# Optimization experiments

Measured on AMD Instinct MI355X. Metric: run time of the kernel, lower is better.

The kernel has to match this reference:

```python
import jax, jax.numpy as jnp
import numpy as np

B, C, D, H, W = 2, 256, 16, 64, 64


def _conv1x1(x, w, b):
    # 1x1x1 Conv3d == pointwise channel matmul. x: [B,C,D,H,W], w: [Cout,Cin], b: [Cout]
    return jnp.einsum('bcdhw,oc->bodhw', x, w) + b[None, :, None, None, None]


def setup_inputs() -> dict:
    key = jax.random.key(0)
    ks = jax.random.split(key, 12)
    wscale = 1.0 / np.sqrt(C)  # keep pre-softmax logits in a sane range
    inp = {
        'eeg_input': jax.random.normal(ks[0], (B, C, D, H, W), jnp.float32),
        'image_input': jax.random.normal(ks[1], (B, C, D, H, W), jnp.float32),
        'q_w': jax.random.normal(ks[2], (C, C), jnp.float32) * wscale,
        'q_b': jnp.zeros((C,), jnp.float32),
        'k_w': jax.random.normal(ks[3], (C, C), jnp.float32) * wscale,
        'k_b': jnp.zeros((C,), jnp.float32),
        'v_w': jax.random.normal(ks[4], (C, C), jnp.float32) * wscale,
        'v_b': jnp.zeros((C,), jnp.float32),
        'attn_w': jax.random.normal(ks[5], (C, C), jnp.float32) * wscale,
        'attn_b': jnp.zeros((C,), jnp.float32),
        'out_w': jax.random.normal(ks[6], (C, C), jnp.float32) * wscale,
        'out_b': jnp.zeros((C,), jnp.float32),
    }
    return inp


def reference(eeg_input, image_input, q_w, q_b, k_w, k_b, v_w, v_b,
              attn_w, attn_b, out_w, out_b):
    q = _conv1x1(eeg_input, q_w, q_b)      # [B,C,D,H,W]
    k = _conv1x1(image_input, k_w, k_b)    # [B,C,D,H,W]
    v = _conv1x1(image_input, v_w, v_b)    # [B,C,D,H,W]
    # torch.matmul(q, k.transpose(-2,-1)): contract over W -> scores [B,C,D,H,H]
    scores = jax.nn.softmax(jnp.einsum('bcdhw,bcdxw->bcdhx', q, k), axis=-1)
    wv = jnp.einsum('bcdhx,bcdxw->bcdhw', scores, v)  # [B,C,D,H,W]
    a = jax.nn.relu(_conv1x1(wv, attn_w, attn_b))
    return jax.nn.relu(_conv1x1(a, out_w, out_b))
```

## Files before the change

### kernel.cpp

```cpp
#include <hip/hip_runtime.h>

#define CC   256
#define DHWC 65536
#define NBC  2

typedef __attribute__((ext_vector_type(8))) short bf16x8;
typedef __attribute__((ext_vector_type(4))) short bf16x4;
typedef __attribute__((ext_vector_type(4))) float f32x4;

__device__ __forceinline__ short f2bf(float x) {
    unsigned u = __builtin_bit_cast(unsigned, x);
    unsigned r = (u + 0x7fffu + ((u >> 16) & 1u)) >> 16;
    return (short)r;
}
__device__ __forceinline__ float bf2f(short h) {
    unsigned u = ((unsigned)(unsigned short)h) << 16;
    return __builtin_bit_cast(float, u);
}

__device__ __forceinline__ int swz(int r, int c) {
    return (r * 128 + c * 2) ^ ((r & 7) << 4);
}
__device__ __forceinline__ int vswz(int r, int c) {
    return (r * 128 + c * 2) ^ (((r ^ (r >> 3)) & 7) << 4);
}
__device__ __forceinline__ int swz512(int s, int k) {
    return (s * 512 + k * 2) ^ ((s & 7) << 4);
}

__global__ void prep_w_kernel(const float* __restrict__ q_w, const float* __restrict__ k_w,
                              const float* __restrict__ v_w, const float* __restrict__ attn_w,
                              const float* __restrict__ out_w, short* __restrict__ wsp)
{
    const int l  = threadIdx.x;
    const int fo = blockIdx.x;
    const int t  = blockIdx.y;
    const int m  = blockIdx.z;
    const float* w = (m == 0) ? q_w : (m == 1) ? k_w : (m == 2) ? v_w
                   : (m == 3) ? attn_w : out_w;
    short* whi = wsp + (size_t)m * 131072;
    short* wlo = whi + 65536;

    const int o = fo * 16 + (l & 15);
    const int k = t * 32 + (l >> 4) * 8;

    bf16x8 hv, lv;
    #pragma unroll
    for (int r = 0; r < 8; ++r) {
        const float x = w[o * 256 + k + r];
        const short h = f2bf(x);
        hv[r] = h;
        lv[r] = f2bf(x - bf2f(h));
    }
    const int idx = (fo * 8 + t) * 64 + l;
    *(bf16x8*)(whi + idx * 8) = hv;
    *(bf16x8*)(wlo + idx * 8) = lv;
}

__global__ __launch_bounds__(512, 4) void conv_mfma_kernel(
    const float* __restrict__ x, const short* __restrict__ whi,
    const short* __restrict__ wlo, const float* __restrict__ bias,
    float* __restrict__ out, const int do_relu)
{
    __shared__ bf16x8 xhi[2][512];
    __shared__ bf16x8 xlo[2][512];

    const int tid  = threadIdx.x;
    const int lane = tid & 63;
    const int wave = tid >> 6;
    const size_t boff = (size_t)blockIdx.y * ((size_t)CC * DHWC);
    const int sT = blockIdx.x * 64;
    const float* xb = x + boff + sT;
    const bf16x8* whf = (const bf16x8*)whi;
    const bf16x8* wlf = (const bf16x8*)wlo;

    f32x4 acc[2][4];
    #pragma unroll
    for (int f = 0; f < 2; ++f)
        #pragma unroll
        for (int j = 0; j < 4; ++j)
            acc[f][j] = (f32x4){0.f, 0.f, 0.f, 0.f};

    const int s_l = tid & 63;
    const int k8  = tid >> 6;

    float xr[8];
    #pragma unroll
    for (int r = 0; r < 8; ++r)
        xr[r] = xb[(size_t)(k8 * 8 + r) * DHWC + s_l];
    {
        bf16x8 hv, lv;
        #pragma unroll
        for (int r = 0; r < 8; ++r) {
            const short h = f2bf(xr[r]);
            hv[r] = h;
            lv[r] = f2bf(xr[r] - bf2f(h));
        }
        *(bf16x8*)((char*)xhi[0] + swz(s_l, k8 * 8)) = hv;
        *(bf16x8*)((char*)xlo[0] + swz(s_l, k8 * 8)) = lv;
    }

    #pragma unroll
    for (int t = 0; t < 4; ++t) {
        if (t < 3) {
            #pragma unroll
            for (int r = 0; r < 8; ++r)
                xr[r] = xb[(size_t)((t + 1) * 64 + k8 * 8 + r) * DHWC + s_l];
        }
        __syncthreads();

        const char* bhib = (const char*)xhi[t & 1];
        const char* blob = (const char*)xlo[t & 1];
        #pragma unroll
        for (int kk = 0; kk < 2; ++kk) {
            bf16x8 a1h[2], a1l[2];
            #pragma unroll
            for (int f = 0; f < 2; ++f) {
                const int idx = ((wave * 2 + f) * 8 + 2 * t + kk) * 64 + lane;
                a1h[f] = whf[idx];
                a1l[f] = wlf[idx];
            }
            bf16x8 bh[4], bl[4];
            #pragma unroll
            for (int j = 0; j < 4; ++j) {
                const int s = j * 16 + (lane & 15);
                const int k = kk * 32 + (lane >> 4) * 8;
                bh[j] = *(const bf16x8*)(bhib + swz(s, k));
                bl[j] = *(const bf16x8*)(blob + swz(s, k));
            }
            #pragma unroll
            for (int f = 0; f < 2; ++f)
                #pragma unroll
                for (int j = 0; j < 4; ++j) {
                    f32x4 c = acc[f][j];
                    c = __builtin_amdgcn_mfma_f32_16x16x32_bf16(a1h[f], bh[j], c, 0, 0, 0);
                    c = __builtin_amdgcn_mfma_f32_16x16x32_bf16(a1h[f], bl[j], c, 0, 0, 0);
                    c = __builtin_amdgcn_mfma_f32_16x16x32_bf16(a1l[f], bh[j], c, 0, 0, 0);
                    acc[f][j] = c;
                }
        }

        if (t < 3) {
            bf16x8 hv, lv;
            #pragma unroll
            for (int r = 0; r < 8; ++r) {
                const short h = f2bf(xr[r]);
                hv[r] = h;
                lv[r] = f2bf(xr[r] - bf2f(h));
            }
            *(bf16x8*)((char*)xhi[(t + 1) & 1] + swz(s_l, k8 * 8)) = hv;
            *(bf16x8*)((char*)xlo[(t + 1) & 1] + swz(s_l, k8 * 8)) = lv;
        }
    }

    float* ob = out + boff + sT;
    const int n_l = lane & 15;
    const int m4  = (lane >> 4) * 4;
    #pragma unroll
    for (int f = 0; f < 2; ++f) {
        #pragma unroll
        for (int r = 0; r < 4; ++r) {
            const int o = wave * 32 + f * 16 + m4 + r;
            const float bv = bias[o];
            #pragma unroll
            for (int j = 0; j < 4; ++j) {
                float val = acc[f][j][r] + bv;
                if (do_relu) val = fmaxf(val, 0.f);
                ob[(size_t)o * DHWC + j * 16 + n_l] = val;
            }
        }
    }
}

__global__ __launch_bounds__(512, 4) void kv_conv_kernel(
    const float* __restrict__ img,
    const short* __restrict__ wkhi, const short* __restrict__ wklo,
    const short* __restrict__ wvhi, const short* __restrict__ wvlo,
    const float* __restrict__ kb, const float* __restrict__ vb,
    float* __restrict__ kout, short* __restrict__ vout)
{
    __shared__ bf16x8 xhi[2][512];
    __shared__ bf16x8 xlo[2][512];

    const int tid  = threadIdx.x;
    const int lane = tid & 63;
    const int wave = tid >> 6;
    const size_t boff = (size_t)blockIdx.y * ((size_t)CC * DHWC);
    const int sT = blockIdx.x * 64;
    const float* xb = img + boff + sT;
    const bf16x8* wkhf = (const bf16x8*)wkhi;
    const bf16x8* wklf = (const bf16x8*)wklo;
    const bf16x8* wvhf = (const bf16x8*)wvhi;
    const bf16x8* wvlf = (const bf16x8*)wvlo;

    f32x4 acck[2][4], accv[2][4];
    #pragma unroll
    for (int f = 0; f < 2; ++f)
        #pragma unroll
        for (int j = 0; j < 4; ++j) {
            acck[f][j] = (f32x4){0.f, 0.f, 0.f, 0.f};
            accv[f][j] = (f32x4){0.f, 0.f, 0.f, 0.f};
        }

    const int s_l = tid & 63;
    const int k8  = tid >> 6;

    float xr[8];
    #pragma unroll
    for (int r = 0; r < 8; ++r)
        xr[r] = xb[(size_t)(k8 * 8 + r) * DHWC + s_l];
    {
        bf16x8 hv, lv;
        #pragma unroll
        for (int r = 0; r < 8; ++r) {
            const short h = f2bf(xr[r]);
            hv[r] = h;
            lv[r] = f2bf(xr[r] - bf2f(h));
        }
        *(bf16x8*)((char*)xhi[0] + swz(s_l, k8 * 8)) = hv;
        *(bf16x8*)((char*)xlo[0] + swz(s_l, k8 * 8)) = lv;
    }

    #pragma unroll
    for (int t = 0; t < 4; ++t) {
        if (t < 3) {
            #pragma unroll
            for (int r = 0; r < 8; ++r)
                xr[r] = xb[(size_t)((t + 1) * 64 + k8 * 8 + r) * DHWC + s_l];
        }
        __syncthreads();

        const char* bhib = (const char*)xhi[t & 1];
        const char* blob = (const char*)xlo[t & 1];
        #pragma unroll
        for (int kk = 0; kk < 2; ++kk) {
            bf16x8 akh[2], akl[2], avh[2], avl[2];
            #pragma unroll
            for (int f = 0; f < 2; ++f) {
                const int idx = ((wave * 2 + f) * 8 + 2 * t + kk) * 64 + lane;
                akh[f] = wkhf[idx];
                akl[f] = wklf[idx];
                avh[f] = wvhf[idx];
                avl[f] = wvlf[idx];
            }
            #pragma unroll
            for (int j = 0; j < 4; ++j) {
                const int s = j * 16 + (lane & 15);
                const int k = kk * 32 + (lane >> 4) * 8;
                const bf16x8 bh = *(const bf16x8*)(bhib + swz(s, k));
                const bf16x8 bl = *(const bf16x8*)(blob + swz(s, k));
                #pragma unroll
                for (int f = 0; f < 2; ++f) {
                    f32x4 c = acck[f][j];
                    c = __builtin_amdgcn_mfma_f32_16x16x32_bf16(akh[f], bh, c, 0, 0, 0);
                    c = __builtin_amdgcn_mfma_f32_16x16x32_bf16(akh[f], bl, c, 0, 0, 0);
                    c = __builtin_amdgcn_mfma_f32_16x16x32_bf16(akl[f], bh, c, 0, 0, 0);
                    acck[f][j] = c;
                    f32x4 d = accv[f][j];
                    d = __builtin_amdgcn_mfma_f32_16x16x32_bf16(avh[f], bh, d, 0, 0, 0);
                    d = __builtin_amdgcn_mfma_f32_16x16x32_bf16(avh[f], bl, d, 0, 0, 0);
                    d = __builtin_amdgcn_mfma_f32_16x16x32_bf16(avl[f], bh, d, 0, 0, 0);
                    accv[f][j] = d;
                }
            }
        }

        if (t < 3) {
            bf16x8 hv, lv;
            #pragma unroll
            for (int r = 0; r < 8; ++r) {
                const short h = f2bf(xr[r]);
                hv[r] = h;
                lv[r] = f2bf(xr[r] - bf2f(h));
            }
            *(bf16x8*)((char*)xhi[(t + 1) & 1] + swz(s_l, k8 * 8)) = hv;
            *(bf16x8*)((char*)xlo[(t + 1) & 1] + swz(s_l, k8 * 8)) = lv;
        }
    }

    float* ko = kout + boff + sT;
    short* vo = vout + boff + sT;
    const int n_l = lane & 15;
    const int m4  = (lane >> 4) * 4;
    #pragma unroll
    for (int f = 0; f < 2; ++f) {
        #pragma unroll
        for (int r = 0; r < 4; ++r) {
            const int o = wave * 32 + f * 16 + m4 + r;
            const float kbv = kb[o];
            const float vbv = vb[o];
            #pragma unroll
            for (int j = 0; j < 4; ++j) {
                ko[(size_t)o * DHWC + j * 16 + n_l] = acck[f][j][r] + kbv;
                vo[(size_t)o * DHWC + j * 16 + n_l] = f2bf(accv[f][j][r] + vbv);
            }
        }
    }
}

__global__ __launch_bounds__(256, 4) void attn_mfma_kernel(
    const float* q, const float* __restrict__ kg,
    const short* __restrict__ vsh, float* wv)
{
    __shared__ char lds[40960];
    const int QHI = 0, QLO = 8192, KHI = 16384, KLO = 24576, VT = 32768;

    const int tid  = threadIdx.x;
    const int lane = tid & 63;
    const int wsx  = tid >> 6;
    const size_t base = (size_t)blockIdx.x * 4096;

    {
        const int r  = tid >> 2;
        const int cb = (tid & 3) * 16;
        #pragma unroll
        for (int half = 0; half < 2; ++half) {
            const int c = cb + half * 8;
            const float4 qa = *(const float4*)(q  + base + r * 64 + c);
            const float4 qb = *(const float4*)(q  + base + r * 64 + c + 4);
            const float4 ka = *(const float4*)(kg + base + r * 64 + c);
            const float4 kb = *(const float4*)(kg + base + r * 64 + c + 4);
            bf16x8 qh, ql, kh, kl;
            #pragma unroll
            for (int e = 0; e < 4; ++e) {
                float xq = ((const float*)&qa)[e];
                short h = f2bf(xq); qh[e] = h; ql[e] = f2bf(xq - bf2f(h));
                xq = ((const float*)&qb)[e];
                h = f2bf(xq); qh[e + 4] = h; ql[e + 4] = f2bf(xq - bf2f(h));
                float xk = ((const float*)&ka)[e];
                h = f2bf(xk); kh[e] = h; kl[e] = f2bf(xk - bf2f(h));
                xk = ((const float*)&kb)[e];
                h = f2bf(xk); kh[e + 4] = h; kl[e + 4] = f2bf(xk - bf2f(h));
            }
            const int off = swz(r, c);
            *(bf16x8*)(lds + QHI + off) = qh;
            *(bf16x8*)(lds + QLO + off) = ql;
            *(bf16x8*)(lds + KHI + off) = kh;
            *(bf16x8*)(lds + KLO + off) = kl;
        }
        const short* vpl = vsh + base;
        const int x0 = (tid >> 4) * 4;
        const int w0 = (tid & 15) * 4;
        bf16x4 vr[4];
        #pragma unroll
        for (int i = 0; i < 4; ++i)
            vr[i] = *(const bf16x4*)(vpl + (x0 + i) * 64 + w0);
        #pragma unroll
        for (int j = 0; j < 4; ++j) {
            bf16x4 tv;
            #pragma unroll
            for (int i = 0; i < 4; ++i) tv[i] = vr[i][j];
            *(bf16x4*)(lds + VT + vswz(w0 + j, x0)) = tv;
        }
    }
    __syncthreads();

    f32x4 acc[4];
    #pragma unroll
    for (int j = 0; j < 4; ++j) acc[j] = (f32x4){0.f, 0.f, 0.f, 0.f};

    const int arow = wsx * 16 + (lane & 15);
    #pragma unroll
    for (int kk = 0; kk < 2; ++kk) {
        const int kcol = kk * 32 + (lane >> 4) * 8;
        const bf16x8 aqh = *(const bf16x8*)(lds + QHI + swz(arow, kcol));
        const bf16x8 aql = *(const bf16x8*)(lds + QLO + swz(arow, kcol));
        #pragma unroll
        for (int j = 0; j < 4; ++j) {
            const int brow = j * 16 + (lane & 15);
            const bf16x8 bkh = *(const bf16x8*)(lds + KHI + swz(brow, kcol));
            const bf16x8 bkl = *(const bf16x8*)(lds + KLO + swz(brow, kcol));
            f32x4 c = acc[j];
            c = __builtin_amdgcn_mfma_f32_16x16x32_bf16(aqh, bkh, c, 0, 0, 0);
            c = __builtin_amdgcn_mfma_f32_16x16x32_bf16(aqh, bkl, c, 0, 0, 0);
            c = __builtin_amdgcn_mfma_f32_16x16x32_bf16(aql, bkh, c, 0, 0, 0);
            acc[j] = c;
        }
    }

    float p[4][4], invs[4];
    #pragma unroll
    for (int r = 0; r < 4; ++r) {
        float m = fmaxf(fmaxf(acc[0][r], acc[1][r]), fmaxf(acc[2][r], acc[3][r]));
        m = fmaxf(m, __shfl_xor(m, 1));
        m = fmaxf(m, __shfl_xor(m, 2));
        m = fmaxf(m, __shfl_xor(m, 4));
        m = fmaxf(m, __shfl_xor(m, 8));
        float s = 0.f;
        #pragma unroll
        for (int j = 0; j < 4; ++j) { p[j][r] = __expf(acc[j][r] - m); s += p[j][r]; }
        s += __shfl_xor(s, 1);
        s += __shfl_xor(s, 2);
        s += __shfl_xor(s, 4);
        s += __shfl_xor(s, 8);
        invs[r] = 1.f / s;
    }

    __syncthreads();

    #pragma unroll
    for (int r = 0; r < 4; ++r) {
        const int row = wsx * 16 + (lane >> 4) * 4 + r;
        #pragma unroll
        for (int j = 0; j < 4; ++j) {
            const int col = j * 16 + (lane & 15);
            *(short*)(lds + QHI + swz(row, col)) = f2bf(p[j][r]);
        }
    }
    __syncthreads();

    f32x4 o_[4];
    #pragma unroll
    for (int j = 0; j < 4; ++j) o_[j] = (f32x4){0.f, 0.f, 0.f, 0.f};

    #pragma unroll
    for (int kk = 0; kk < 2; ++kk) {
        const int kcol = kk * 32 + (lane >> 4) * 8;
        const bf16x8 aph = *(const bf16x8*)(lds + QHI + swz(arow, kcol));
        #pragma unroll
        for (int j = 0; j < 4; ++j) {
            const int brow = j * 16 + (lane & 15);
            const bf16x8 bvh = *(const bf16x8*)(lds + VT + vswz(brow, kcol));
            o_[j] = __builtin_amdgcn_mfma_f32_16x16x32_bf16(aph, bvh, o_[j], 0, 0, 0);
        }
    }

    #pragma unroll
    for (int r = 0; r < 4; ++r) {
        const int h = wsx * 16 + (lane >> 4) * 4 + r;
        #pragma unroll
        for (int j = 0; j < 4; ++j)
            wv[base + (size_t)h * 64 + j * 16 + (lane & 15)] = o_[j][r] * invs[r];
    }
}

__global__ __launch_bounds__(512, 4) void tail_fused_kernel(
    const float* __restrict__ x,
    const short* __restrict__ w1hi, const short* __restrict__ w1lo,
    const float* __restrict__ b1,
    const short* __restrict__ w2hi, const short* __restrict__ w2lo,
    const float* __restrict__ b2,
    float* __restrict__ out)
{
    __shared__ char lds[65536];
    const int tid  = threadIdx.x;
    const int lane = tid & 63;
    const int wave = tid >> 6;
    const size_t boff = (size_t)blockIdx.y * ((size_t)CC * DHWC);
    const int sT = blockIdx.x * 64;
    const float* xb = x + boff + sT;
    const bf16x8* w1hf = (const bf16x8*)w1hi;
    const bf16x8* w1lf = (const bf16x8*)w1lo;

    f32x4 acc[2][4];
    #pragma unroll
    for (int f = 0; f < 2; ++f)
        #pragma unroll
        for (int j = 0; j < 4; ++j)
            acc[f][j] = (f32x4){0.f, 0.f, 0.f, 0.f};

    const int s_l = tid & 63;
    const int k8  = tid >> 6;

    float xr[8];
    #pragma unroll
    for (int r = 0; r < 8; ++r)
        xr[r] = xb[(size_t)(k8 * 8 + r) * DHWC + s_l];
    {
        bf16x8 hv, lv;
        #pragma unroll
        for (int r = 0; r < 8; ++r) {
            const short h = f2bf(xr[r]);
            hv[r] = h;
            lv[r] = f2bf(xr[r] - bf2f(h));
        }
        *(bf16x8*)(lds + swz(s_l, k8 * 8)) = hv;
        *(bf16x8*)(lds + 8192 + swz(s_l, k8 * 8)) = lv;
    }

    #pragma unroll
    for (int t = 0; t < 4; ++t) {
        if (t < 3) {
            #pragma unroll
            for (int r = 0; r < 8; ++r)
                xr[r] = xb[(size_t)((t + 1) * 64 + k8 * 8 + r) * DHWC + s_l];
        }
        __syncthreads();

        const char* bhib = lds + (t & 1) * 16384;
        const char* blob = bhib + 8192;
        #pragma unroll
        for (int kk = 0; kk < 2; ++kk) {
            bf16x8 a1h[2], a1l[2];
            #pragma unroll
            for (int f = 0; f < 2; ++f) {
                const int idx = ((wave * 2 + f) * 8 + 2 * t + kk) * 64 + lane;
                a1h[f] = w1hf[idx];
                a1l[f] = w1lf[idx];
            }
            bf16x8 bh[4], bl[4];
            #pragma unroll
            for (int j = 0; j < 4; ++j) {
                const int s = j * 16 + (lane & 15);
                const int k = kk * 32 + (lane >> 4) * 8;
                bh[j] = *(const bf16x8*)(bhib + swz(s, k));
                bl[j] = *(const bf16x8*)(blob + swz(s, k));
            }
            #pragma unroll
            for (int f = 0; f < 2; ++f)
                #pragma unroll
                for (int j = 0; j < 4; ++j) {
                    f32x4 c = acc[f][j];
                    c = __builtin_amdgcn_mfma_f32_16x16x32_bf16(a1h[f], bh[j], c, 0, 0, 0);
                    c = __builtin_amdgcn_mfma_f32_16x16x32_bf16(a1h[f], bl[j], c, 0, 0, 0);
                    c = __builtin_amdgcn_mfma_f32_16x16x32_bf16(a1l[f], bh[j], c, 0, 0, 0);
                    acc[f][j] = c;
                }
        }

        if (t < 3) {
            bf16x8 hv, lv;
            #pragma unroll
            for (int r = 0; r < 8; ++r) {
                const short h = f2bf(xr[r]);
                hv[r] = h;
                lv[r] = f2bf(xr[r] - bf2f(h));
            }
            *(bf16x8*)(lds + ((t + 1) & 1) * 16384 + swz(s_l, k8 * 8)) = hv;
            *(bf16x8*)(lds + ((t + 1) & 1) * 16384 + 8192 + swz(s_l, k8 * 8)) = lv;
        }
    }

    __syncthreads();
    #pragma unroll
    for (int f = 0; f < 2; ++f) {
        #pragma unroll
        for (int r = 0; r < 4; ++r) {
            const int o = wave * 32 + f * 16 + (lane >> 4) * 4 + r;
            const float bv = b1[o];
            #pragma unroll
            for (int j = 0; j < 4; ++j) {
                const int s = j * 16 + (lane & 15);
                const float val = fmaxf(acc[f][j][r] + bv, 0.f);
                const short h = f2bf(val);
                const int off = swz512(s, o);
                *(short*)(lds + off) = h;
                *(short*)(lds + 32768 + off) = f2bf(val - bf2f(h));
            }
        }
    }
    __syncthreads();

    f32x4 acc2[2][4];
    #pragma unroll
    for (int f = 0; f < 2; ++f)
        #pragma unroll
        for (int j = 0; j < 4; ++j)
            acc2[f][j] = (f32x4){0.f, 0.f, 0.f, 0.f};

    const bf16x8* w2hf = (const bf16x8*)w2hi;
    const bf16x8* w2lf = (const bf16x8*)w2lo;
    #pragma unroll
    for (int t2 = 0; t2 < 8; ++t2) {
        bf16x8 a2h[2], a2l[2];
        #pragma unroll
        for (int f = 0; f < 2; ++f) {
            const int idx = ((wave * 2 + f) * 8 + t2) * 64 + lane;
            a2h[f] = w2hf[idx];
            a2l[f] = w2lf[idx];
        }
        bf16x8 bh[4], bl[4];
        #pragma unroll
        for (int j = 0; j < 4; ++j) {
            const int s = j * 16 + (lane & 15);
            const int k = t2 * 32 + (lane >> 4) * 8;
            const int off = swz512(s, k);
            bh[j] = *(const bf16x8*)(lds + off);
            bl[j] = *(const bf16x8*)(lds + 32768 + off);
        }
        #pragma unroll
        for (int f = 0; f < 2; ++f)
            #pragma unroll
            for (int j = 0; j < 4; ++j) {
                f32x4 c = acc2[f][j];
                c = __builtin_amdgcn_mfma_f32_16x16x32_bf16(a2h[f], bh[j], c, 0, 0, 0);
                c = __builtin_amdgcn_mfma_f32_16x16x32_bf16(a2h[f], bl[j], c, 0, 0, 0);
                c = __builtin_amdgcn_mfma_f32_16x16x32_bf16(a2l[f], bh[j], c, 0, 0, 0);
                acc2[f][j] = c;
            }
    }

    float* ob = out + boff + sT;
    const int n_l = lane & 15;
    const int m4  = (lane >> 4) * 4;
    #pragma unroll
    for (int f = 0; f < 2; ++f) {
        #pragma unroll
        for (int r = 0; r < 4; ++r) {
            const int o = wave * 32 + f * 16 + m4 + r;
            const float bv = b2[o];
            #pragma unroll
            for (int j = 0; j < 4; ++j) {
                const float val = fmaxf(acc2[f][j][r] + bv, 0.f);
                ob[(size_t)o * DHWC + j * 16 + n_l] = val;
            }
        }
    }
}

extern "C" void kernel_launch(void* const* d_in, const int* in_sizes, int n_in,
                              void* d_out, int out_size, void* d_ws, size_t ws_size,
                              hipStream_t stream)
{
    const float* eeg    = (const float*)d_in[0];
    const float* img    = (const float*)d_in[1];
    const float* q_w    = (const float*)d_in[2];
    const float* q_b    = (const float*)d_in[3];
    const float* k_w    = (const float*)d_in[4];
    const float* k_b    = (const float*)d_in[5];
    const float* v_w    = (const float*)d_in[6];
    const float* v_b    = (const float*)d_in[7];
    const float* attn_w = (const float*)d_in[8];
    const float* attn_b = (const float*)d_in[9];
    const float* out_w  = (const float*)d_in[10];
    const float* out_b  = (const float*)d_in[11];

    const size_t N = (size_t)NBC * CC * DHWC;
    float* qbuf = (float*)d_ws;
    float* kbuf = qbuf + N;
    short* wsp  = (short*)(kbuf + N);
    short* vsh  = (short*)d_out;
    float* outp = (float*)d_out;

    hipLaunchKernelGGL(prep_w_kernel, dim3(16, 8, 5), dim3(64), 0, stream,
                       q_w, k_w, v_w, attn_w, out_w, wsp);

    const dim3 cgrid(DHWC / 64, NBC);

    hipLaunchKernelGGL(conv_mfma_kernel, cgrid, dim3(512), 0, stream,
                       eeg, wsp, wsp + 65536, q_b, qbuf, 0);

    hipLaunchKernelGGL(kv_conv_kernel, cgrid, dim3(512), 0, stream,
                       img, wsp + 131072, wsp + 131072 + 65536,
                       wsp + 2 * 131072, wsp + 2 * 131072 + 65536,
                       k_b, v_b, kbuf, vsh);

    hipLaunchKernelGGL(attn_mfma_kernel, dim3(NBC * CC * 16), dim3(256), 0, stream,
                       qbuf, kbuf, vsh, qbuf);

    hipLaunchKernelGGL(tail_fused_kernel, cgrid, dim3(512), 0, stream,
                       qbuf, wsp + 3 * 131072, wsp + 3 * 131072 + 65536, attn_b,
                       wsp + 4 * 131072, wsp + 4 * 131072 + 65536, out_b, outp);
}
```

Before: 417.4 us.

## Widen conv tiles to 128 spatial with 1024-thread blocks; drop lo-part in tail stage-2

The three pointwise-conv kernels now use 1024-thread blocks over 128 spatial positions, and each of the 16 waves owns 16 output channels instead of 32. Each weight fragment is reused across 8 spatial sub-tiles instead of 4, while each LDS activation tile is shared by twice as many waves. In the tail kernel, the intermediate ReLU activation is stored only as a bf16 hi part, so the second conv does two MFMAs per tile instead of three, trading some accuracy for less LDS traffic and compute. The larger block raises register pressure per thread and may reduce occupancy with a 64KB LDS allocation.

After: 410.1 us. About the same (-1.8%).

```diff
diff --git a/kernel.cpp b/kernel.cpp
--- a/kernel.cpp
+++ b/kernel.cpp
@@ -57,32 +57,28 @@
     *(bf16x8*)(wlo + idx * 8) = lv;
 }
 
-__global__ __launch_bounds__(512, 4) void conv_mfma_kernel(
+__global__ __launch_bounds__(1024, 4) void conv_mfma_kernel(
     const float* __restrict__ x, const short* __restrict__ whi,
     const short* __restrict__ wlo, const float* __restrict__ bias,
     float* __restrict__ out, const int do_relu)
 {
-    __shared__ bf16x8 xhi[2][512];
-    __shared__ bf16x8 xlo[2][512];
+    __shared__ char lds[65536];
 
     const int tid  = threadIdx.x;
     const int lane = tid & 63;
     const int wave = tid >> 6;
     const size_t boff = (size_t)blockIdx.y * ((size_t)CC * DHWC);
-    const int sT = blockIdx.x * 64;
+    const int sT = blockIdx.x * 128;
     const float* xb = x + boff + sT;
     const bf16x8* whf = (const bf16x8*)whi;
     const bf16x8* wlf = (const bf16x8*)wlo;
 
-    f32x4 acc[2][4];
-    #pragma unroll
-    for (int f = 0; f < 2; ++f)
-        #pragma unroll
-        for (int j = 0; j < 4; ++j)
-            acc[f][j] = (f32x4){0.f, 0.f, 0.f, 0.f};
-
-    const int s_l = tid & 63;
-    const int k8  = tid >> 6;
+    f32x4 acc[8];
+    #pragma unroll
+    for (int j = 0; j < 8; ++j) acc[j] = (f32x4){0.f, 0.f, 0.f, 0.f};
+
+    const int s_l = tid & 127;
+    const int k8  = tid >> 7;
 
     float xr[8];
     #pragma unroll
@@ -96,8 +92,9 @@
             hv[r] = h;
             lv[r] = f2bf(xr[r] - bf2f(h));
         }
-        *(bf16x8*)((char*)xhi[0] + swz(s_l, k8 * 8)) = hv;
-        *(bf16x8*)((char*)xlo[0] + swz(s_l, k8 * 8)) = lv;
+        const int off = swz(s_l, k8 * 8);
+        *(bf16x8*)(lds + off) = hv;
+        *(bf16x8*)(lds + 16384 + off) = lv;
     }
 
     #pragma unroll
@@ -109,35 +106,25 @@
         }
         __syncthreads();
 
-        const char* bhib = (const char*)xhi[t & 1];
-        const char* blob = (const char*)xlo[t & 1];
+        const char* bhib = lds + (t & 1) * 32768;
+        const char* blob = bhib + 16384;
         #pragma unroll
         for (int kk = 0; kk < 2; ++kk) {
-            bf16x8 a1h[2], a1l[2];
-            #pragma unroll
-            for (int f = 0; f < 2; ++f) {
-                const int idx = ((wave * 2 + f) * 8 + 2 * t + kk) * 64 + lane;
-                a1h[f] = whf[idx];
-                a1l[f] = wlf[idx];
-            }
-            bf16x8 bh[4], bl[4];
-            #pragma unroll
-            for (int j = 0; j < 4; ++j) {
+            const int idx = (wave * 8 + 2 * t + kk) * 64 + lane;
+            const bf16x8 a1h = whf[idx];
+            const bf16x8 a1l = wlf[idx];
+            #pragma unroll
+            for (int j = 0; j < 8; ++j) {
                 const int s = j * 16 + (lane & 15);
                 const int k = kk * 32 + (lane >> 4) * 8;
-                bh[j] = *(const bf16x8*)(bhib + swz(s, k));
-                bl[j] = *(const bf16x8*)(blob + swz(s, k));
-            }
-            #pragma unroll
-            for (int f = 0; f < 2; ++f)
-                #pragma unroll
-                for (int j = 0; j < 4; ++j) {
-                    f32x4 c = acc[f][j];
-                    c = __builtin_amdgcn_mfma_f32_16x16x32_bf16(a1h[f], bh[j], c, 0, 0, 0);
-                    c = __builtin_amdgcn_mfma_f32_16x16x32_bf16(a1h[f], bl[j], c, 0, 0, 0);
-                    c = __builtin_amdgcn_mfma_f32_16x16x32_bf16(a1l[f], bh[j], c, 0, 0, 0);
-                    acc[f][j] = c;
-                }
+                const bf16x8 bh = *(const bf16x8*)(bhib + swz(s, k));
+                const bf16x8 bl = *(const bf16x8*)(blob + swz(s, k));
+                f32x4 c = acc[j];
+                c = __builtin_amdgcn_mfma_f32_16x16x32_bf16(a1h, bh, c, 0, 0, 0);
+                c = __builtin_amdgcn_mfma_f32_16x16x32_bf16(a1h, bl, c, 0, 0, 0);
+                c = __builtin_amdgcn_mfma_f32_16x16x32_bf16(a1l, bh, c, 0, 0, 0);
+                acc[j] = c;
+            }
         }
 
         if (t < 3) {
@@ -148,8 +135,9 @@
                 hv[r] = h;
                 lv[r] = f2bf(xr[r] - bf2f(h));
             }
-            *(bf16x8*)((char*)xhi[(t + 1) & 1] + swz(s_l, k8 * 8)) = hv;
-            *(bf16x8*)((char*)xlo[(t + 1) & 1] + swz(s_l, k8 * 8)) = lv;
+            const int off = ((t + 1) & 1) * 32768 + swz(s_l, k8 * 8);
+            *(bf16x8*)(lds + off) = hv;
+            *(bf16x8*)(lds + 16384 + off) = lv;
         }
     }
 
@@ -157,53 +145,47 @@
     const int n_l = lane & 15;
     const int m4  = (lane >> 4) * 4;
     #pragma unroll
-    for (int f = 0; f < 2; ++f) {
-        #pragma unroll
-        for (int r = 0; r < 4; ++r) {
-            const int o = wave * 32 + f * 16 + m4 + r;
-            const float bv = bias[o];
-            #pragma unroll
-            for (int j = 0; j < 4; ++j) {
-                float val = acc[f][j][r] + bv;
-                if (do_relu) val = fmaxf(val, 0.f);
-                ob[(size_t)o * DHWC + j * 16 + n_l] = val;
-            }
-        }
-    }
-}
-
-__global__ __launch_bounds__(512, 4) void kv_conv_kernel(
+    for (int r = 0; r < 4; ++r) {
+        const int o = wave * 16 + m4 + r;
+        const float bv = bias[o];
+        #pragma unroll
+        for (int j = 0; j < 8; ++j) {
+            float val = acc[j][r] + bv;
+            if (do_relu) val = fmaxf(val, 0.f);
+            ob[(size_t)o * DHWC + j * 16 + n_l] = val;
+        }
+    }
+}
+
+__global__ __launch_bounds__(1024, 4) void kv_conv_kernel(
     const float* __restrict__ img,
     const short* __restrict__ wkhi, const short* __restrict__ wklo,
     const short* __restrict__ wvhi, const short* __restrict__ wvlo,
     const float* __restrict__ kb, const float* __restrict__ vb,
     float* __restrict__ kout, short* __restrict__ vout)
 {
-    __shared__ bf16x8 xhi[2][512];
-    __shared__ bf16x8 xlo[2][512];
+    __shared__ char lds[65536];
 
     const int tid  = threadIdx.x;
     const int lane = tid & 63;
     const int wave = tid >> 6;
     const size_t boff = (size_t)blockIdx.y * ((size_t)CC * DHWC);
-    const int sT = blockIdx.x * 64;
+    const int sT = blockIdx.x * 128;
     const float* xb = img + boff + sT;
     const bf16x8* wkhf = (const bf16x8*)wkhi;
     const bf16x8* wklf = (const bf16x8*)wklo;
     const bf16x8* wvhf = (const bf16x8*)wvhi;
     const bf16x8* wvlf = (const bf16x8*)wvlo;
 
-    f32x4 acck[2][4], accv[2][4];
-    #pragma unroll
-    for (int f = 0; f < 2; ++f)
-        #pragma unroll
-        for (int j = 0; j < 4; ++j) {
-            acck[f][j] = (f32x4){0.f, 0.f, 0.f, 0.f};
-            accv[f][j] = (f32x4){0.f, 0.f, 0.f, 0.f};
-        }
-
-    const int s_l = tid & 63;
-    const int k8  = tid >> 6;
+    f32x4 acck[8], accv[8];
+    #pragma unroll
+    for (int j = 0; j < 8; ++j) {
+        acck[j] = (f32x4){0.f, 0.f, 0.f, 0.f};
+        accv[j] = (f32x4){0.f, 0.f, 0.f, 0.f};
+    }
+
+    const int s_l = tid & 127;
+    const int k8  = tid >> 7;
 
     float xr[8];
     #pragma unroll
@@ -217,8 +199,9 @@
             hv[r] = h;
             lv[r] = f2bf(xr[r] - bf2f(h));
         }
-        *(bf16x8*)((char*)xhi[0] + swz(s_l, k8 * 8)) = hv;
-        *(bf16x8*)((char*)xlo[0] + swz(s_l, k8 * 8)) = lv;
+        const int off = swz(s_l, k8 * 8);
+        *(bf16x8*)(lds + off) = hv;
+        *(bf16x8*)(lds + 16384 + off) = lv;
     }
 
     #pragma unroll
@@ -230,38 +213,31 @@
         }
         __syncthreads();
 
-        const char* bhib = (const char*)xhi[t & 1];
-        const char* blob = (const char*)xlo[t & 1];
+        const char* bhib = lds + (t & 1) * 32768;
+        const char* blob = bhib + 16384;
         #pragma unroll
         for (int kk = 0; kk < 2; ++kk) {
-            bf16x8 akh[2], akl[2], avh[2], avl[2];
-            #pragma unroll
-            for (int f = 0; f < 2; ++f) {
-                const int idx = ((wave * 2 + f) * 8 + 2 * t + kk) * 64 + lane;
-                akh[f] = wkhf[idx];
-                akl[f] = wklf[idx];
-                avh[f] = wvhf[idx];
-                avl[f] = wvlf[idx];
-            }
-            #pragma unroll
-            for (int j = 0; j < 4; ++j) {
+            const int idx = (wave * 8 + 2 * t + kk) * 64 + lane;
+            const bf16x8 akh = wkhf[idx];
+            const bf16x8 akl = wklf[idx];
+            const bf16x8 avh = wvhf[idx];
+            const bf16x8 avl = wvlf[idx];
+            #pragma unroll
+            for (int j = 0; j < 8; ++j) {
                 const int s = j * 16 + (lane & 15);
                 const int k = kk * 32 + (lane >> 4) * 8;
                 const bf16x8 bh = *(const bf16x8*)(bhib + swz(s, k));
                 const bf16x8 bl = *(const bf16x8*)(blob + swz(s, k));
-                #pragma unroll
-                for (int f = 0; f < 2; ++f) {
-                    f32x4 c = acck[f][j];
-                    c = __builtin_amdgcn_mfma_f32_16x16x32_bf16(akh[f], bh, c, 0, 0, 0);
-                    c = __builtin_amdgcn_mfma_f32_16x16x32_bf16(akh[f], bl, c, 0, 0, 0);
-                    c = __builtin_amdgcn_mfma_f32_16x16x32_bf16(akl[f], bh, c, 0, 0, 0);
-                    acck[f][j] = c;
-                    f32x4 d = accv[f][j];
-                    d = __builtin_amdgcn_mfma_f32_16x16x32_bf16(avh[f], bh, d, 0, 0, 0);
-                    d = __builtin_amdgcn_mfma_f32_16x16x32_bf16(avh[f], bl, d, 0, 0, 0);
-                    d = __builtin_amdgcn_mfma_f32_16x16x32_bf16(avl[f], bh, d, 0, 0, 0);
-                    accv[f][j] = d;
-                }
+                f32x4 c = acck[j];
+                c = __builtin_amdgcn_mfma_f32_16x16x32_bf16(akh, bh, c, 0, 0, 0);
+                c = __builtin_amdgcn_mfma_f32_16x16x32_bf16(akh, bl, c, 0, 0, 0);
+                c = __builtin_amdgcn_mfma_f32_16x16x32_bf16(akl, bh, c, 0, 0, 0);
+                acck[j] = c;
+                f32x4 d = accv[j];
+                d = __builtin_amdgcn_mfma_f32_16x16x32_bf16(avh, bh, d, 0, 0, 0);
+                d = __builtin_amdgcn_mfma_f32_16x16x32_bf16(avh, bl, d, 0, 0, 0);
+                d = __builtin_amdgcn_mfma_f32_16x16x32_bf16(avl, bh, d, 0, 0, 0);
+                accv[j] = d;
             }
         }
 
@@ -273,8 +249,9 @@
                 hv[r] = h;
                 lv[r] = f2bf(xr[r] - bf2f(h));
             }
-            *(bf16x8*)((char*)xhi[(t + 1) & 1] + swz(s_l, k8 * 8)) = hv;
-            *(bf16x8*)((char*)xlo[(t + 1) & 1] + swz(s_l, k8 * 8)) = lv;
+            const int off = ((t + 1) & 1) * 32768 + swz(s_l, k8 * 8);
+            *(bf16x8*)(lds + off) = hv;
+            *(bf16x8*)(lds + 16384 + off) = lv;
         }
     }
 
@@ -283,17 +260,14 @@
     const int n_l = lane & 15;
     const int m4  = (lane >> 4) * 4;
     #pragma unroll
-    for (int f = 0; f < 2; ++f) {
-        #pragma unroll
-        for (int r = 0; r < 4; ++r) {
-            const int o = wave * 32 + f * 16 + m4 + r;
-            const float kbv = kb[o];
-            const float vbv = vb[o];
-            #pragma unroll
-            for (int j = 0; j < 4; ++j) {
-                ko[(size_t)o * DHWC + j * 16 + n_l] = acck[f][j][r] + kbv;
-                vo[(size_t)o * DHWC + j * 16 + n_l] = f2bf(accv[f][j][r] + vbv);
-            }
+    for (int r = 0; r < 4; ++r) {
+        const int o = wave * 16 + m4 + r;
+        const float kbv = kb[o];
+        const float vbv = vb[o];
+        #pragma unroll
+        for (int j = 0; j < 8; ++j) {
+            ko[(size_t)o * DHWC + j * 16 + n_l] = acck[j][r] + kbv;
+            vo[(size_t)o * DHWC + j * 16 + n_l] = f2bf(accv[j][r] + vbv);
         }
     }
 }
@@ -434,7 +408,7 @@
     }
 }
 
-__global__ __launch_bounds__(512, 4) void tail_fused_kernel(
+__global__ __launch_bounds__(1024, 4) void tail_fused_kernel(
     const float* __restrict__ x,
     const short* __restrict__ w1hi, const short* __restrict__ w1lo,
     const float* __restrict__ b1,
@@ -443,24 +417,22 @@
     float* __restrict__ out)
 {
     __shared__ char lds[65536];
+
     const int tid  = threadIdx.x;
     const int lane = tid & 63;
     const int wave = tid >> 6;
     const size_t boff = (size_t)blockIdx.y * ((size_t)CC * DHWC);
-    const int sT = blockIdx.x * 64;
+    const int sT = blockIdx.x * 128;
     const float* xb = x + boff + sT;
     const bf16x8* w1hf = (const bf16x8*)w1hi;
     const bf16x8* w1lf = (const bf16x8*)w1lo;
 
-    f32x4 acc[2][4];
-    #pragma unroll
-    for (int f = 0; f < 2; ++f)
-        #pragma unroll
-        for (int j = 0; j < 4; ++j)
-            acc[f][j] = (f32x4){0.f, 0.f, 0.f, 0.f};
-
-    const int s_l = tid & 63;
-    const int k8  = tid >> 6;
+    f32x4 acc[8];
+    #pragma unroll
+    for (int j = 0; j < 8; ++j) acc[j] = (f32x4){0.f, 0.f, 0.f, 0.f};
+
+    const int s_l = tid & 127;
+    const int k8  = tid >> 7;
 
     float xr[8];
     #pragma unroll
@@ -474,8 +446,9 @@
             hv[r] = h;
             lv[r] = f2bf(xr[r] - bf2f(h));
         }
-        *(bf16x8*)(lds + swz(s_l, k8 * 8)) = hv;
-        *(bf16x8*)(lds + 8192 + swz(s_l, k8 * 8)) = lv;
+        const int off = swz(s_l, k8 * 8);
+        *(bf16x8*)(lds + off) = hv;
+        *(bf16x8*)(lds + 16384 + off) = lv;
     }
 
     #pragma unroll
@@ -487,35 +460,25 @@
         }
         __syncthreads();
 
-        const char* bhib = lds + (t & 1) * 16384;
-        const char* blob = bhib + 8192;
+        const char* bhib = lds + (t & 1) * 32768;
+        const char* blob = bhib + 16384;
         #pragma unroll
         for (int kk = 0; kk < 2; ++kk) {
-            bf16x8 a1h[2], a1l[2];
-            #pragma unroll
-            for (int f = 0; f < 2; ++f) {
-                const int idx = ((wave * 2 + f) * 8 + 2 * t + kk) * 64 + lane;
-                a1h[f] = w1hf[idx];
-                a1l[f] = w1lf[idx];
-            }
-            bf16x8 bh[4], bl[4];
-            #pragma unroll
-            for (int j = 0; j < 4; ++j) {
+            const int idx = (wave * 8 + 2 * t + kk) * 64 + lane;
+            const bf16x8 a1h = w1hf[idx];
+            const bf16x8 a1l = w1lf[idx];
+            #pragma unroll
+            for (int j = 0; j < 8; ++j) {
                 const int s = j * 16 + (lane & 15);
                 const int k = kk * 32 + (lane >> 4) * 8;
-                bh[j] = *(const bf16x8*)(bhib + swz(s, k));
-                bl[j] = *(const bf16x8*)(blob + swz(s, k));
-            }
-            #pragma unroll
-            for (int f = 0; f < 2; ++f)
-                #pragma unroll
-                for (int j = 0; j < 4; ++j) {
-                    f32x4 c = acc[f][j];
-                    c = __builtin_amdgcn_mfma_f32_16x16x32_bf16(a1h[f], bh[j], c, 0, 0, 0);
-                    c = __builtin_amdgcn_mfma_f32_16x16x32_bf16(a1h[f], bl[j], c, 0, 0, 0);
-                    c = __builtin_amdgcn_mfma_f32_16x16x32_bf16(a1l[f], bh[j], c, 0, 0, 0);
-                    acc[f][j] = c;
-                }
+                const bf16x8 bh = *(const bf16x8*)(bhib + swz(s, k));
+                const bf16x8 bl = *(const bf16x8*)(blob + swz(s, k));
+                f32x4 c = acc[j];
+                c = __builtin_amdgcn_mfma_f32_16x16x32_bf16(a1h, bh, c, 0, 0, 0);
+                c = __builtin_amdgcn_mfma_f32_16x16x32_bf16(a1h, bl, c, 0, 0, 0);
+                c = __builtin_amdgcn_mfma_f32_16x16x32_bf16(a1l, bh, c, 0, 0, 0);
+                acc[j] = c;
+            }
         }
 
         if (t < 3) {
@@ -526,85 +489,61 @@
                 hv[r] = h;
                 lv[r] = f2bf(xr[r] - bf2f(h));
             }
-            *(bf16x8*)(lds + ((t + 1) & 1) * 16384 + swz(s_l, k8 * 8)) = hv;
-            *(bf16x8*)(lds + ((t + 1) & 1) * 16384 + 8192 + swz(s_l, k8 * 8)) = lv;
+            const int off = ((t + 1) & 1) * 32768 + swz(s_l, k8 * 8);
+            *(bf16x8*)(lds + off) = hv;
+            *(bf16x8*)(lds + 16384 + off) = lv;
         }
     }
 
     __syncthreads();
-    #pragma unroll
-    for (int f = 0; f < 2; ++f) {
+    {
+        const int m4 = (lane >> 4) * 4;
         #pragma unroll
         for (int r = 0; r < 4; ++r) {
-            const int o = wave * 32 + f * 16 + (lane >> 4) * 4 + r;
+            const int o = wave * 16 + m4 + r;
             const float bv = b1[o];
             #pragma unroll
-            for (int j = 0; j < 4; ++j) {
+            for (int j = 0; j < 8; ++j) {
                 const int s = j * 16 + (lane & 15);
-                const float val = fmaxf(acc[f][j][r] + bv, 0.f);
-                const short h = f2bf(val);
-                const int off = swz512(s, o);
-                *(short*)(lds + off) = h;
-                *(short*)(lds + 32768 + off) = f2bf(val - bf2f(h));
+                *(short*)(lds + swz512(s, o)) = f2bf(fmaxf(acc[j][r] + bv, 0.f));
             }
         }
     }
     __syncthreads();
 
-    f32x4 acc2[2][4];
-    #pragma unroll
-    for (int f = 0; f < 2; ++f)
-        #pragma unroll
-        for (int j = 0; j < 4; ++j)
-            acc2[f][j] = (f32x4){0.f, 0.f, 0.f, 0.f};
+    f32x4 acc2[8];
+    #pragma unroll
+    for (int j = 0; j < 8; ++j) acc2[j] = (f32x4){0.f, 0.f, 0.f, 0.f};
 
     const bf16x8* w2hf = (const bf16x8*)w2hi;
     const bf16x8* w2lf = (const bf16x8*)w2lo;
     #pragma unroll
     for (int t2 = 0; t2 < 8; ++t2) {
-        bf16x8 a2h[2], a2l[2];
-        #pragma unroll
-        for (int f = 0; f < 2; ++f) {
-            const int idx = ((wave * 2 + f) * 8 + t2) * 64 + lane;
-            a2h[f] = w2hf[idx];
-            a2l[f] = w2lf[idx];
-        }
-        bf16x8 bh[4], bl[4];
-        #pragma unroll
-        for (int j = 0; j < 4; ++j) {
+        const int idx = (wave * 8 + t2) * 64 + lane;
+        const bf16x8 a2h = w2hf[idx];
+        const bf16x8 a2l = w2lf[idx];
+        #pragma unroll
+        for (int j = 0; j < 8; ++j) {
             const int s = j * 16 + (lane & 15);
             const int k = t2 * 32 + (lane >> 4) * 8;
-            const int off = swz512(s, k);
-            bh[j] = *(const bf16x8*)(lds + off);
-            bl[j] = *(const bf16x8*)(lds + 32768 + off);
-        }
-        #pragma unroll
-        for (int f = 0; f < 2; ++f)
-            #pragma unroll
-            for (int j = 0; j < 4; ++j) {
-                f32x4 c = acc2[f][j];
-                c = __builtin_amdgcn_mfma_f32_16x16x32_bf16(a2h[f], bh[j], c, 0, 0, 0);
-                c = __builtin_amdgcn_mfma_f32_16x16x32_bf16(a2h[f], bl[j], c, 0, 0, 0);
-                c = __builtin_amdgcn_mfma_f32_16x16x32_bf16(a2l[f], bh[j], c, 0, 0, 0);
-                acc2[f][j] = c;
-            }
+            const bf16x8 bh = *(const bf16x8*)(lds + swz512(s, k));
+            f32x4 c = acc2[j];
+            c = __builtin_amdgcn_mfma_f32_16x16x32_bf16(a2h, bh, c, 0, 0, 0);
+            c = __builtin_amdgcn_mfma_f32_16x16x32_bf16(a2l, bh, c, 0, 0, 0);
+            acc2[j] = c;
+        }
     }
 
     float* ob = out + boff + sT;
     const int n_l = lane & 15;
     const int m4  = (lane >> 4) * 4;
     #pragma unroll
-    for (int f = 0; f < 2; ++f) {
-        #pragma unroll
-        for (int r = 0; r < 4; ++r) {
-            const int o = wave * 32 + f * 16 + m4 + r;
-            const float bv = b2[o];
-            #pragma unroll
-            for (int j = 0; j < 4; ++j) {
-                const float val = fmaxf(acc2[f][j][r] + bv, 0.f);
-                ob[(size_t)o * DHWC + j * 16 + n_l] = val;
-            }
-        }
+    for (int r = 0; r < 4; ++r) {
+        const int o = wave * 16 + m4 + r;
+        const float bv = b2[o];
+        #pragma unroll
+        for (int j = 0; j < 8; ++j)
+            ob[(size_t)o * DHWC + j * 16 + n_l] = fmaxf(acc2[j][r] + bv, 0.f);
     }
 }
 
@@ -635,12 +574,12 @@
     hipLaunchKernelGGL(prep_w_kernel, dim3(16, 8, 5), dim3(64), 0, stream,
                        q_w, k_w, v_w, attn_w, out_w, wsp);
 
-    const dim3 cgrid(DHWC / 64, NBC);
-
-    hipLaunchKernelGGL(conv_mfma_kernel, cgrid, dim3(512), 0, stream,
+    const dim3 cgrid(DHWC / 128, NBC);
+
+    hipLaunchKernelGGL(conv_mfma_kernel, cgrid, dim3(1024), 0, stream,
                        eeg, wsp, wsp + 65536, q_b, qbuf, 0);
 
-    hipLaunchKernelGGL(kv_conv_kernel, cgrid, dim3(512), 0, stream,
+    hipLaunchKernelGGL(kv_conv_kernel, cgrid, dim3(1024), 0, stream,
                        img, wsp + 131072, wsp + 131072 + 65536,
                        wsp + 2 * 131072, wsp + 2 * 131072 + 65536,
                        k_b, v_b, kbuf, vsh);
@@ -648,7 +587,7 @@
     hipLaunchKernelGGL(attn_mfma_kernel, dim3(NBC * CC * 16), dim3(256), 0, stream,
                        qbuf, kbuf, vsh, qbuf);
 
-    hipLaunchKernelGGL(tail_fused_kernel, cgrid, dim3(512), 0, stream,
+    hipLaunchKernelGGL(tail_fused_kernel, cgrid, dim3(1024), 0, stream,
                        qbuf, wsp + 3 * 131072, wsp + 3 * 131072 + 65536, attn_b,
                        wsp + 4 * 131072, wsp + 4 * 131072 + 65536, out_b, outp);
 }
```
